# Optimization experiments

Hardware: AMD Instinct MI355X
Metric: run time of the kernel (lower is better)

## Reference

```python
import jax, jax.numpy as jnp
import numpy as np

N, E = 8192, 256
NUM_CLASSES = 4
MARGIN = 0.5
EPS = 1e-8  # torch F.cosine_similarity eps


def setup_inputs() -> dict:
    key = jax.random.key(0)
    k1, k2 = jax.random.split(key)
    inp = jax.random.normal(k1, (N, E), dtype=jnp.float32)
    target = jax.random.randint(k2, (N,), 0, NUM_CLASSES, dtype=jnp.int64)
    return {"input": inp, "target": target}


def reference(input, target):
    n, e = input.shape
    # cosine similarity via normalized matmul (QK^T style) instead of O(N^2 E) broadcast
    norm = jnp.maximum(jnp.linalg.norm(input, axis=1), EPS)
    xn = input / norm[:, None]                      # [N, E]
    cossim = xn @ xn.T                              # [N, N]

    triu = jnp.triu(jnp.ones((n, n), dtype=bool), k=1)  # strict upper triangle

    # initial same_class_mask from binary target; overwritten in the loop below
    binary = target > 0
    same_class_mask = binary[:, None] == binary[None, :]

    same_class_loss = jnp.zeros((), dtype=input.dtype)
    for i in range(NUM_CLASSES):
        is_i = target == i
        cnt = jnp.sum(is_i).astype(input.dtype)
        mask_i = is_i[:, None] == is_i[None, :]     # matches (target==i) vs (target==i) outer equality
        # torch computes target_a == target_b with both being (target==i):
        # equal when both True OR both False
        term = jnp.sum((1.0 - cossim) * (mask_i & triu).astype(input.dtype))
        same_class_loss = same_class_loss + jnp.where(
            cnt > 0, term / jnp.maximum(cnt, 1.0), 0.0
        )
        # torch's loop leaves same_class_mask equal to the last class with counts > 0
        same_class_mask = jnp.where(cnt > 0, mask_i, same_class_mask)

    diff = jax.nn.relu(cossim * (~same_class_mask).astype(input.dtype) - MARGIN)
    diff_class_loss = jnp.sum(diff * triu.astype(input.dtype))

    return (same_class_loss + diff_class_loss) / n
```

## Files before the change

### kernel.cpp

```cpp
#include <hip/hip_runtime.h>

#define NROWS 8192
#define EDIM  256
#define NB    64
#define NPAIR 2080
#define BKB   64
#define NCHUNK 8
#define PART_OFF 256
#define XN_OFF   16384

typedef __bf16 bf16x8 __attribute__((ext_vector_type(8)));
typedef float  f32x4  __attribute__((ext_vector_type(4)));

__device__ __forceinline__ unsigned short f2bf(float f) {
  unsigned int u = __float_as_uint(f);
  u += 0x7fffu + ((u >> 16) & 1u);
  return (unsigned short)(u >> 16);
}

__device__ __forceinline__ void gl_lds16(const void* g, void* l) {
  __builtin_amdgcn_global_load_lds(
      (const __attribute__((address_space(1))) unsigned int*)g,
      (__attribute__((address_space(3))) unsigned int*)l, 16, 0, 0);
}

__global__ __launch_bounds__(256) void k_norm(const float* __restrict__ x,
                                              unsigned short* __restrict__ xn) {
  int row  = blockIdx.x * 4 + (threadIdx.x >> 6);
  int lane = threadIdx.x & 63;
  float4 v = reinterpret_cast<const float4*>(x)[row * 64 + lane];
  float ss = v.x * v.x + v.y * v.y + v.z * v.z + v.w * v.w;
#pragma unroll
  for (int off = 32; off; off >>= 1) ss += __shfl_xor(ss, off);
  float inv = 1.0f / fmaxf(sqrtf(ss), 1e-8f);
  ushort4 o;
  o.x = f2bf(v.x * inv); o.y = f2bf(v.y * inv);
  o.z = f2bf(v.z * inv); o.w = f2bf(v.w * inv);
  reinterpret_cast<ushort4*>(xn)[row * 64 + lane] = o;
}

__global__ __launch_bounds__(256) void k_hist(const int* __restrict__ t,
                                              int* __restrict__ cnt) {
  __shared__ int lc[4];
  if (threadIdx.x < 4) lc[threadIdx.x] = 0;
  __syncthreads();
  int i = blockIdx.x * 256 + threadIdx.x;
  atomicAdd(&lc[t[i]], 1);
  __syncthreads();
  if (threadIdx.x < 4) atomicAdd(&cnt[threadIdx.x], lc[threadIdx.x]);
}

__global__ __launch_bounds__(256, 4) void k_main(const unsigned short* __restrict__ xn,
                                                 const int* __restrict__ tgt,
                                                 const int* __restrict__ cnt,
                                                 float* __restrict__ partial) {
  __shared__ char  lds[2][2][128 * BKB];
  __shared__ int   ltrow[128], ltcol[128];
  __shared__ float lW[16];
  __shared__ int   lsL;
  __shared__ float wred[4];

  int bid0 = blockIdx.x;
  int bid  = (bid0 & 7) * (NPAIR / 8) + (bid0 >> 3);

  int r = 0, rem = bid;
  while (rem >= NB - r) { rem -= NB - r; ++r; }
  int cb = r + rem;

  const int tid = threadIdx.x;
  const int wave = tid >> 6, lane = tid & 63;

  const char* xb   = (const char*)xn;
  const char* srcA = xb + (size_t)r  * 128 * 512;
  const char* srcB = xb + (size_t)cb * 128 * 512;

  auto stage = [&](int buf, int chunk) {
    int slot16 = (lane & 3) * 16;
#pragma unroll
    for (int i = 0; i < 2; ++i) {
      int rbase = i * 64 + wave * 16;
      int row   = rbase + (lane >> 2);
      int key   = ((row >> 1) & 3) << 4;
      size_t go = (size_t)row * 512 + chunk * BKB + (slot16 ^ key);
      gl_lds16(srcA + go, &lds[buf][0][rbase * BKB]);
      gl_lds16(srcB + go, &lds[buf][1][rbase * BKB]);
    }
  };

  stage(0, 0);

  if (tid < 128) { ltrow[tid] = tgt[r * 128 + tid]; ltcol[tid] = tgt[cb * 128 + tid]; }
  if (tid < 16) {
    int ta = tid >> 2, tb = tid & 3;
    float w = 0.0f;
#pragma unroll
    for (int i = 0; i < 4; ++i) {
      int ci = cnt[i];
      if (ci > 0 && ((ta == i) == (tb == i))) w += 1.0f / (float)ci;
    }
    lW[tid] = w;
  }
  if (tid == 0) {
    int L = -1;
    for (int i = 0; i < 4; ++i) if (cnt[i] > 0) L = i;
    lsL = L;
  }
  __syncthreads();

  const int wr = (wave >> 1) * 64, wc = (wave & 1) * 64;
  f32x4 acc[4][4];
#pragma unroll
  for (int m = 0; m < 4; ++m)
#pragma unroll
    for (int n = 0; n < 4; ++n)
      acc[m][n] = (f32x4){0.f, 0.f, 0.f, 0.f};

  const int l15 = lane & 15;
  const int kb_lane = (lane >> 4) << 4;

  int cur = 0;
  for (int c = 0; c < NCHUNK; ++c) {
    if (c + 1 < NCHUNK) stage(cur ^ 1, c + 1);

    const char* cA = lds[cur][0];
    const char* cB = lds[cur][1];
    bf16x8 af[4], bfr[4];
#pragma unroll
    for (int m = 0; m < 4; ++m) {
      int arow = wr + m * 16 + l15;
      af[m] = *reinterpret_cast<const bf16x8*>(cA + arow * BKB + (kb_lane ^ (((arow >> 1) & 3) << 4)));
    }
#pragma unroll
    for (int n = 0; n < 4; ++n) {
      int brow = wc + n * 16 + l15;
      bfr[n] = *reinterpret_cast<const bf16x8*>(cB + brow * BKB + (kb_lane ^ (((brow >> 1) & 3) << 4)));
    }
#pragma unroll
    for (int m = 0; m < 4; ++m)
#pragma unroll
      for (int n = 0; n < 4; ++n)
        acc[m][n] = __builtin_amdgcn_mfma_f32_16x16x32_bf16(af[m], bfr[n], acc[m][n], 0, 0, 0);

    __syncthreads();
    cur ^= 1;
  }

  const int L = lsL;
  float lsum = 0.0f;
  const int rowj = (lane >> 4) * 4;
#pragma unroll
  for (int m = 0; m < 4; ++m) {
#pragma unroll
    for (int n = 0; n < 4; ++n) {
#pragma unroll
      for (int j = 0; j < 4; ++j) {
        int ar = wr + m * 16 + rowj + j;
        int bc = wc + n * 16 + l15;
        int ga = r * 128 + ar, gb = cb * 128 + bc;
        if (ga < gb) {
          float cv = acc[m][n][j];
          int ta = ltrow[ar], tb = ltcol[bc];
          float contrib = lW[ta * 4 + tb] * (1.0f - cv);
          if ((ta == L) != (tb == L)) contrib += fmaxf(cv - 0.5f, 0.0f);
          lsum += contrib;
        }
      }
    }
  }
#pragma unroll
  for (int off = 32; off; off >>= 1) lsum += __shfl_xor(lsum, off);
  if (lane == 0) wred[wave] = lsum;
  __syncthreads();
  if (tid == 0) partial[bid] = wred[0] + wred[1] + wred[2] + wred[3];
}

__global__ __launch_bounds__(256) void k_reduce(const float* __restrict__ partial,
                                                float* __restrict__ out) {
  __shared__ float red[4];
  int tid = threadIdx.x, wave = tid >> 6, lane = tid & 63;
  float s = 0.0f;
  for (int i = tid; i < NPAIR; i += 256) s += partial[i];
#pragma unroll
  for (int off = 32; off; off >>= 1) s += __shfl_xor(s, off);
  if (lane == 0) red[wave] = s;
  __syncthreads();
  if (tid == 0) out[0] = (red[0] + red[1] + red[2] + red[3]) * (1.0f / 8192.0f);
}

extern "C" void kernel_launch(void* const* d_in, const int* in_sizes, int n_in,
                              void* d_out, int out_size, void* d_ws, size_t ws_size,
                              hipStream_t stream) {
  (void)in_sizes; (void)n_in; (void)out_size; (void)ws_size;
  const float* x  = (const float*)d_in[0];
  const int* tgt  = (const int*)d_in[1];
  float* out      = (float*)d_out;
  int* cnt        = (int*)d_ws;
  float* partial  = (float*)((char*)d_ws + PART_OFF);
  unsigned short* xn = (unsigned short*)((char*)d_ws + XN_OFF);

  hipMemsetAsync(cnt, 0, 4 * sizeof(int), stream);
  k_norm<<<NROWS / 4, 256, 0, stream>>>(x, xn);
  k_hist<<<NROWS / 256, 256, 0, stream>>>(tgt, cnt);
  k_main<<<NPAIR, 256, 0, stream>>>(xn, tgt, cnt, partial);
  k_reduce<<<1, 256, 0, stream>>>(partial, out);
}
```

Measured before the change: 59.32 us.

## Make k_main persistent over segments of tile pairs, keeping A row-block resident

```diff
diff --git a/kernel.cpp b/kernel.cpp
--- a/kernel.cpp
+++ b/kernel.cpp
@@ -1,11 +1,9 @@
 #include <hip/hip_runtime.h>
 
 #define NROWS 8192
-#define EDIM  256
 #define NB    64
 #define NPAIR 2080
-#define BKB   64
-#define NCHUNK 8
+#define NSEG  512
 #define PART_OFF 256
 #define XN_OFF   16384
 
@@ -50,46 +48,86 @@
   if (threadIdx.x < 4) atomicAdd(&cnt[threadIdx.x], lc[threadIdx.x]);
 }
 
-__global__ __launch_bounds__(256, 4) void k_main(const unsigned short* __restrict__ xn,
+__global__ __launch_bounds__(256, 1) void k_main(const unsigned short* __restrict__ xn,
                                                  const int* __restrict__ tgt,
                                                  const int* __restrict__ cnt,
                                                  float* __restrict__ partial) {
-  __shared__ char  lds[2][2][128 * BKB];
-  __shared__ int   ltrow[128], ltcol[128];
+  __shared__ __align__(16) char lA[8 * 128 * 64];
+  __shared__ __align__(16) char lB[2][4 * 128 * 64];
   __shared__ float lW[16];
   __shared__ int   lsL;
   __shared__ float wred[4];
 
-  int bid0 = blockIdx.x;
-  int bid  = (bid0 & 7) * (NPAIR / 8) + (bid0 >> 3);
-
-  int r = 0, rem = bid;
+  int b0 = blockIdx.x;
+  int s  = (b0 & 7) * (NSEG / 8) + (b0 >> 3);
+  int nlong_before = (s + 15) >> 4;
+  int start = 4 * s + nlong_before;
+  int n     = 4 + ((s & 15) == 0 ? 1 : 0);
+  int r = 0, rem = start;
   while (rem >= NB - r) { rem -= NB - r; ++r; }
   int cb = r + rem;
 
-  const int tid = threadIdx.x;
-  const int wave = tid >> 6, lane = tid & 63;
-
-  const char* xb   = (const char*)xn;
-  const char* srcA = xb + (size_t)r  * 128 * 512;
-  const char* srcB = xb + (size_t)cb * 128 * 512;
-
-  auto stage = [&](int buf, int chunk) {
-    int slot16 = (lane & 3) * 16;
-#pragma unroll
-    for (int i = 0; i < 2; ++i) {
-      int rbase = i * 64 + wave * 16;
-      int row   = rbase + (lane >> 2);
-      int key   = ((row >> 1) & 3) << 4;
-      size_t go = (size_t)row * 512 + chunk * BKB + (slot16 ^ key);
-      gl_lds16(srcA + go, &lds[buf][0][rbase * BKB]);
-      gl_lds16(srcB + go, &lds[buf][1][rbase * BKB]);
+  const int tid = threadIdx.x, wave = tid >> 6, lane = tid & 63;
+  const char* xb = (const char*)xn;
+
+  auto stageA = [&](int rr) {
+    const char* src = xb + (size_t)rr * 128 * 512;
+    int slot = (lane & 3) * 16;
+#pragma unroll
+    for (int it = 0; it < 16; ++it) {
+      int g = it * 4 + wave;
+      int ksub = g >> 3, rbase = (g & 7) * 16;
+      int row  = rbase + (lane >> 2);
+      int key  = ((row >> 1) & 3) << 4;
+      gl_lds16(src + (size_t)row * 512 + ksub * 64 + (slot ^ key),
+               &lA[ksub * 8192 + rbase * 64]);
     }
   };
-
-  stage(0, 0);
-
-  if (tid < 128) { ltrow[tid] = tgt[r * 128 + tid]; ltcol[tid] = tgt[cb * 128 + tid]; }
+  auto stageB = [&](int buf, int cc, int h) {
+    const char* src = xb + (size_t)cc * 128 * 512 + h * 256;
+    int slot = (lane & 3) * 16;
+#pragma unroll
+    for (int it = 0; it < 8; ++it) {
+      int g = it * 4 + wave;
+      int ksub = g >> 3, rbase = (g & 7) * 16;
+      int row  = rbase + (lane >> 2);
+      int key  = ((row >> 1) & 3) << 4;
+      gl_lds16(src + (size_t)row * 512 + ksub * 64 + (slot ^ key),
+               &lB[buf][ksub * 8192 + rbase * 64]);
+    }
+  };
+
+  const int wr = (wave >> 1) * 64, wc = (wave & 1) * 64;
+  const int l15 = lane & 15;
+  const int q16 = (lane >> 4) << 4;
+  const int rowj = (lane >> 4) * 4;
+
+  auto compute = [&](int buf, int h, f32x4 (&acc)[4][4]) {
+    const char* cB = lB[buf];
+#pragma unroll
+    for (int ks = 0; ks < 4; ++ks) {
+      bf16x8 af[4], bfr[4];
+      int ksA = h * 4 + ks;
+#pragma unroll
+      for (int m = 0; m < 4; ++m) {
+        int a = wr + m * 16 + l15;
+        af[m] = *(const bf16x8*)(lA + ksA * 8192 + a * 64 + (q16 ^ (((a >> 1) & 3) << 4)));
+      }
+#pragma unroll
+      for (int nn = 0; nn < 4; ++nn) {
+        int b = wc + nn * 16 + l15;
+        bfr[nn] = *(const bf16x8*)(cB + ks * 8192 + b * 64 + (q16 ^ (((b >> 1) & 3) << 4)));
+      }
+#pragma unroll
+      for (int m = 0; m < 4; ++m)
+#pragma unroll
+        for (int nn = 0; nn < 4; ++nn)
+          acc[m][nn] = __builtin_amdgcn_mfma_f32_16x16x32_bf16(af[m], bfr[nn], acc[m][nn], 0, 0, 0);
+    }
+  };
+
+  stageA(r);
+  stageB(0, cb, 0);
   if (tid < 16) {
     int ta = tid >> 2, tb = tid & 3;
     float w = 0.0f;
@@ -106,80 +144,82 @@
     lsL = L;
   }
   __syncthreads();
-
-  const int wr = (wave >> 1) * 64, wc = (wave & 1) * 64;
-  f32x4 acc[4][4];
-#pragma unroll
-  for (int m = 0; m < 4; ++m)
-#pragma unroll
-    for (int n = 0; n < 4; ++n)
-      acc[m][n] = (f32x4){0.f, 0.f, 0.f, 0.f};
-
-  const int l15 = lane & 15;
-  const int kb_lane = (lane >> 4) << 4;
-
+  const int L = lsL;
+
+  float lsum = 0.0f;
   int cur = 0;
-  for (int c = 0; c < NCHUNK; ++c) {
-    if (c + 1 < NCHUNK) stage(cur ^ 1, c + 1);
-
-    const char* cA = lds[cur][0];
-    const char* cB = lds[cur][1];
-    bf16x8 af[4], bfr[4];
-#pragma unroll
-    for (int m = 0; m < 4; ++m) {
-      int arow = wr + m * 16 + l15;
-      af[m] = *reinterpret_cast<const bf16x8*>(cA + arow * BKB + (kb_lane ^ (((arow >> 1) & 3) << 4)));
-    }
-#pragma unroll
-    for (int n = 0; n < 4; ++n) {
-      int brow = wc + n * 16 + l15;
-      bfr[n] = *reinterpret_cast<const bf16x8*>(cB + brow * BKB + (kb_lane ^ (((brow >> 1) & 3) << 4)));
-    }
+  for (int i = 0; i < n; ++i) {
+    f32x4 acc[4][4];
 #pragma unroll
     for (int m = 0; m < 4; ++m)
 #pragma unroll
-      for (int n = 0; n < 4; ++n)
-        acc[m][n] = __builtin_amdgcn_mfma_f32_16x16x32_bf16(af[m], bfr[n], acc[m][n], 0, 0, 0);
-
+      for (int nn = 0; nn < 4; ++nn)
+        acc[m][nn] = (f32x4){0.f, 0.f, 0.f, 0.f};
+
+    stageB(cur ^ 1, cb, 1);
+    compute(cur, 0, acc);
     __syncthreads();
     cur ^= 1;
+
+    int ncb = cb + 1, nr = r, nrow = 0;
+    if (ncb == NB) { nr = r + 1; ncb = nr; nrow = 1; }
+    int have = (i + 1 < n);
+    if (have && !nrow) stageB(cur ^ 1, ncb, 0);
+    compute(cur, 1, acc);
+    __syncthreads();
+    cur ^= 1;
+
+    {
+      const int rg = r * 128 + wr;
+      const int cg = cb * 128 + wc;
+      int tb[4], tbl[4];
+#pragma unroll
+      for (int nn = 0; nn < 4; ++nn) {
+        tb[nn] = tgt[cg + nn * 16 + l15];
+        tbl[nn] = (tb[nn] == L);
+      }
+#pragma unroll
+      for (int m = 0; m < 4; ++m) {
+#pragma unroll
+        for (int j = 0; j < 4; ++j) {
+          int ar = m * 16 + rowj + j;
+          int ta = tgt[rg + ar];
+          int tal = (ta == L);
+          int ga = rg + ar;
+#pragma unroll
+          for (int nn = 0; nn < 4; ++nn) {
+            int gb = cg + nn * 16 + l15;
+            if (ga < gb) {
+              float cv = acc[m][nn][j];
+              float contrib = lW[ta * 4 + tb[nn]] * (1.0f - cv);
+              if (tal != tbl[nn]) contrib += fmaxf(cv - 0.5f, 0.0f);
+              lsum += contrib;
+            }
+          }
+        }
+      }
+    }
+
+    if (have && nrow) {
+      stageA(nr);
+      stageB(cur, ncb, 0);
+      __syncthreads();
+    }
+    cb = ncb; r = nr;
   }
 
-  const int L = lsL;
-  float lsum = 0.0f;
-  const int rowj = (lane >> 4) * 4;
-#pragma unroll
-  for (int m = 0; m < 4; ++m) {
-#pragma unroll
-    for (int n = 0; n < 4; ++n) {
-#pragma unroll
-      for (int j = 0; j < 4; ++j) {
-        int ar = wr + m * 16 + rowj + j;
-        int bc = wc + n * 16 + l15;
-        int ga = r * 128 + ar, gb = cb * 128 + bc;
-        if (ga < gb) {
-          float cv = acc[m][n][j];
-          int ta = ltrow[ar], tb = ltcol[bc];
-          float contrib = lW[ta * 4 + tb] * (1.0f - cv);
-          if ((ta == L) != (tb == L)) contrib += fmaxf(cv - 0.5f, 0.0f);
-          lsum += contrib;
-        }
-      }
-    }
-  }
 #pragma unroll
   for (int off = 32; off; off >>= 1) lsum += __shfl_xor(lsum, off);
   if (lane == 0) wred[wave] = lsum;
   __syncthreads();
-  if (tid == 0) partial[bid] = wred[0] + wred[1] + wred[2] + wred[3];
+  if (tid == 0) partial[s] = wred[0] + wred[1] + wred[2] + wred[3];
 }
 
 __global__ __launch_bounds__(256) void k_reduce(const float* __restrict__ partial,
                                                 float* __restrict__ out) {
   __shared__ float red[4];
   int tid = threadIdx.x, wave = tid >> 6, lane = tid & 63;
-  float s = 0.0f;
-  for (int i = tid; i < NPAIR; i += 256) s += partial[i];
+  float s = partial[tid] + partial[tid + 256];
 #pragma unroll
   for (int off = 32; off; off >>= 1) s += __shfl_xor(s, off);
   if (lane == 0) red[wave] = s;
@@ -201,6 +241,6 @@
   hipMemsetAsync(cnt, 0, 4 * sizeof(int), stream);
   k_norm<<<NROWS / 4, 256, 0, stream>>>(x, xn);
   k_hist<<<NROWS / 256, 256, 0, stream>>>(tgt, cnt);
-  k_main<<<NPAIR, 256, 0, stream>>>(xn, tgt, cnt, partial);
+  k_main<<<NSEG, 256, 0, stream>>>(xn, tgt, cnt, partial);
   k_reduce<<<1, 256, 0, stream>>>(partial, out);
 }
```

Result: slower. 81.44 us (+37.3%).
